# Kernel optimization log

Measured on AMD Instinct MI355X. Metric: run time of the kernel, lower is better.

Reference implementation:

```python
import jax, jax.numpy as jnp
import numpy as np

EMB = 768
HEADS = 8

def setup_inputs() -> dict:
    key = jax.random.key(0)
    ks = jax.random.split(key, 5)
    x = jax.random.normal(ks[0], (8, 2048, EMB), dtype=jnp.float32)
    s = 1.0 / np.sqrt(EMB)
    W_qkv = jax.random.normal(ks[1], (EMB, 3 * EMB), dtype=jnp.float32) * s
    b_qkv = jnp.zeros((3 * EMB,), dtype=jnp.float32)
    W_proj = jax.random.normal(ks[2], (EMB, EMB), dtype=jnp.float32) * s
    b_proj = jnp.zeros((EMB,), dtype=jnp.float32)
    return {"x": x, "W_qkv": W_qkv, "b_qkv": b_qkv, "W_proj": W_proj, "b_proj": b_proj}

def reference(x, W_qkv, b_qkv, W_proj, b_proj):
    B, N, E = x.shape
    H = HEADS
    D = E // H
    qkv = x @ W_qkv + b_qkv  # [B, N, 3E]
    q, k, v = jnp.split(qkv, 3, axis=-1)
    # [B, N, E] -> [B, H, N, D]
    def heads(t):
        return t.reshape(B, N, H, D).transpose(0, 2, 1, 3)
    q, k, v = heads(q), heads(k), heads(v)
    # NOTE: original scales by 1/sqrt(emb_size), not 1/sqrt(head_dim)
    dots = jnp.einsum('bhnd,bhmd->bhnm', q, k) / jnp.sqrt(jnp.float32(E))
    attn = jax.nn.softmax(dots, axis=-1)  # dropout inactive (eval mode)
    out = jnp.einsum('bhnm,bhmd->bhnd', attn, v)
    out = out.transpose(0, 2, 1, 3).reshape(B, N, E)
    return out @ W_proj + b_proj
```

## Files before the change

### kernel.cpp

```cpp
#include <hip/hip_runtime.h>
#include <hip/hip_bf16.h>

typedef __attribute__((ext_vector_type(8))) short bf16x8;
typedef __attribute__((ext_vector_type(4))) short bf16x4;
typedef __attribute__((ext_vector_type(4))) float f32x4;
typedef __attribute__((ext_vector_type(16))) float f32x16;
typedef __attribute__((ext_vector_type(4))) unsigned int uint4v;

__device__ __forceinline__ short f2bf(float f) {
    unsigned int u = __float_as_uint(f);
    u += 0x7FFFu + ((u >> 16) & 1u);
    return (short)(u >> 16);
}

__device__ __forceinline__ unsigned cvtpk(float lo, float hi) {
    unsigned r;
    asm("v_cvt_pk_bf16_f32 %0, %1, %2" : "=v"(r) : "v"(lo), "v"(hi));
    return r;
}

__device__ __forceinline__ void gload_lds16(const void* g, void* l) {
    __builtin_amdgcn_global_load_lds(
        (const __attribute__((address_space(1))) void*)g,
        (__attribute__((address_space(3))) void*)l, 16, 0, 0);
}

__global__ __launch_bounds__(256) void cast_kernel(const float* __restrict__ in,
                                                   short* __restrict__ out, int n4) {
    int i = blockIdx.x * 256 + threadIdx.x;
    if (i >= n4) return;
    const f32x4 v = *(const f32x4*)(in + (size_t)i * 4);
    bf16x4 o;
    o[0] = f2bf(v[0]); o[1] = f2bf(v[1]); o[2] = f2bf(v[2]); o[3] = f2bf(v[3]);
    *(bf16x4*)(out + (size_t)i * 4) = o;
}

__global__ __launch_bounds__(256) void transpose_cast_kernel(const float* __restrict__ W,
                                                             short* __restrict__ WT,
                                                             int R, int C) {
    __shared__ float tile[64][65];
    const int bc = blockIdx.x * 64;
    const int br = blockIdx.y * 64;
    const int t = threadIdx.x;
#pragma unroll
    for (int i = 0; i < 16; ++i) {
        int o = t + 256 * i;
        int r = o >> 6, c = o & 63;
        tile[r][c] = W[(size_t)(br + r) * C + bc + c];
    }
    __syncthreads();
#pragma unroll
    for (int i = 0; i < 16; ++i) {
        int o = t + 256 * i;
        int c = o >> 6, r = o & 63;
        WT[(size_t)(bc + c) * R + br + r] = f2bf(tile[r][c]);
    }
}

__global__ __launch_bounds__(256, 3) void gemm1_kernel(
    const short* __restrict__ A, const short* __restrict__ BT,
    const float* __restrict__ bias,
    short* __restrict__ Qh, short* __restrict__ Kh, short* __restrict__ Vt)
{
    __shared__ short As[128][64];
    __shared__ short Bs[128][64];
    const int K = 768;
    const int t = threadIdx.x;
    const int w = t >> 6, l = t & 63;
    const int wr = w >> 1, wc = w & 1;
    const int lr = l & 15, lg = l >> 4;

    const int srow = w * 32 + (l >> 3);
    const int scol = (l & 7) * 8;
    const short* Ag = A + (size_t)blockIdx.x * 128 * K + (size_t)srow * K + scol;
    const short* Bg = BT + (size_t)blockIdx.y * 128 * K + (size_t)srow * K + scol;

    const f32x4 z4 = {0.f, 0.f, 0.f, 0.f};
    f32x4 acc[4][4];
#pragma unroll
    for (int i = 0; i < 4; ++i)
#pragma unroll
        for (int j = 0; j < 4; ++j) acc[i][j] = z4;

    for (int kt = 0; kt < K; kt += 64) {
#pragma unroll
        for (int i = 0; i < 4; ++i) {
            gload_lds16(Ag + kt + (size_t)(i * 8) * K, &As[w * 32 + i * 8][0]);
            gload_lds16(Bg + kt + (size_t)(i * 8) * K, &Bs[w * 32 + i * 8][0]);
        }
        __syncthreads();
#pragma unroll
        for (int kk = 0; kk < 2; ++kk) {
            bf16x8 af[4], bfr[4];
#pragma unroll
            for (int mi = 0; mi < 4; ++mi)
                af[mi] = *(const bf16x8*)&As[wr * 64 + mi * 16 + lr][kk * 32 + lg * 8];
#pragma unroll
            for (int ni = 0; ni < 4; ++ni)
                bfr[ni] = *(const bf16x8*)&Bs[wc * 64 + ni * 16 + lr][kk * 32 + lg * 8];
#pragma unroll
            for (int mi = 0; mi < 4; ++mi)
#pragma unroll
                for (int ni = 0; ni < 4; ++ni)
                    acc[mi][ni] = __builtin_amdgcn_mfma_f32_16x16x32_bf16(
                        af[mi], bfr[ni], acc[mi][ni], 0, 0, 0);
        }
        __syncthreads();
    }

    const float qs = 0.05205877f;
    const int rb = blockIdx.x * 128 + wr * 64;
    const int cb = blockIdx.y * 128 + wc * 64;
#pragma unroll
    for (int ni = 0; ni < 4; ++ni) {
        const int c = cb + ni * 16 + lr;
        const float bv = bias[c];
        const int which = (c >= 1536) ? 2 : (c >= 768 ? 1 : 0);
        const int cc = c - which * 768;
        const int h = cc / 96;
        const int d = cc - h * 96;
#pragma unroll
        for (int mi = 0; mi < 4; ++mi) {
            const int r0 = rb + mi * 16 + lg * 4;
            const int b = r0 >> 11, n0 = r0 & 2047;
            const int hb = b * 8 + h;
            if (which == 2) {
                bf16x4 pk;
#pragma unroll
                for (int r = 0; r < 4; ++r) pk[r] = f2bf(acc[mi][ni][r] + bv);
                *(bf16x4*)&Vt[((size_t)hb * 96 + d) * 2048 + n0] = pk;
            } else if (which == 1) {
#pragma unroll
                for (int r = 0; r < 4; ++r)
                    Kh[((size_t)hb * 2048 + n0 + r) * 96 + d] = f2bf(acc[mi][ni][r] + bv);
            } else {
#pragma unroll
                for (int r = 0; r < 4; ++r)
                    Qh[((size_t)hb * 2048 + n0 + r) * 96 + d] = f2bf((acc[mi][ni][r] + bv) * qs);
            }
        }
    }
}

__global__ __launch_bounds__(256, 2) void attn_kernel(
    const short* __restrict__ Qh, const short* __restrict__ Kh,
    const short* __restrict__ Vt, short* __restrict__ AO)
{
    __shared__ __align__(16) char smem[54272];
    short (*Ks0)[104] = (short (*)[104])smem;
    short (*Ks1)[104] = (short (*)[104])(smem + 13312);
    short (*Vs0)[72]  = (short (*)[72])(smem + 26624);
    short (*Vs1)[72]  = (short (*)[72])(smem + 40448);
    short (*Qs)[104]  = (short (*)[104])smem;
    float (*ltab)[32] = (float (*)[32])smem;

    const int t = threadIdx.x;
    const int w = t >> 6, l = t & 63;
    const int ql = l & 31, hi = l >> 5;

    const unsigned L = blockIdx.y * 16 + blockIdx.x;
    const int bh = (int)((L & 7) + 8 * (L >> 7));
    const int qt = (int)((L >> 3) & 15);

    const short* Qg = Qh + (size_t)bh * 2048 * 96 + (size_t)qt * 128 * 96;
    const short* Kg = Kh + (size_t)bh * 2048 * 96;
    const short* Vg = Vt + (size_t)bh * 96 * 2048;

    bf16x8 kreg[3], vreg[3];
#pragma unroll
    for (int i = 0; i < 3; ++i) {
        int o = t + 256 * i;
        kreg[i] = *(const bf16x8*)(Kg + 8 * (size_t)o);
        vreg[i] = *(const bf16x8*)(Vg + (size_t)(o >> 3) * 2048 + (o & 7) * 8);
    }

#pragma unroll
    for (int i = 0; i < 6; ++i) {
        int o = t + 256 * i;
        *(bf16x8*)&Qs[o / 12][(o % 12) * 8] = *(const bf16x8*)(Qg + 8 * (size_t)o);
    }
    __syncthreads();
    bf16x8 qf[6];
#pragma unroll
    for (int kk = 0; kk < 6; ++kk)
        qf[kk] = *(const bf16x8*)&Qs[w * 32 + ql][kk * 16 + hi * 8];
    __syncthreads();

#pragma unroll
    for (int i = 0; i < 3; ++i) {
        int o = t + 256 * i;
        *(bf16x8*)&Ks0[o / 12][(o % 12) * 8] = kreg[i];
        *(bf16x8*)&Vs0[o >> 3][(o & 7) * 8] = vreg[i];
    }
#pragma unroll
    for (int i = 0; i < 3; ++i) {
        int o = t + 256 * i;
        kreg[i] = *(const bf16x8*)(Kg + (size_t)64 * 96 + 8 * (size_t)o);
        vreg[i] = *(const bf16x8*)(Vg + (size_t)(o >> 3) * 2048 + 64 + (o & 7) * 8);
    }
    __syncthreads();

    f32x16 oacc[3];
#pragma unroll
    for (int i = 0; i < 3; ++i)
#pragma unroll
        for (int r = 0; r < 16; ++r) oacc[i][r] = 0.f;
    float lacc = 0.f;

    auto iter = [&](int kt, short (*rK)[104], short (*rV)[72],
                    short (*wK)[104], short (*wV)[72]) {
        if (kt < 31) {
#pragma unroll
            for (int i = 0; i < 3; ++i) {
                int o = t + 256 * i;
                *(bf16x8*)&wK[o / 12][(o % 12) * 8] = kreg[i];
                *(bf16x8*)&wV[o >> 3][(o & 7) * 8] = vreg[i];
            }
        }
        if (kt < 30) {
            const size_t koff = (size_t)(kt + 2) * 64 * 96;
            const int moff = (kt + 2) * 64;
#pragma unroll
            for (int i = 0; i < 3; ++i) {
                int o = t + 256 * i;
                kreg[i] = *(const bf16x8*)(Kg + koff + 8 * (size_t)o);
                vreg[i] = *(const bf16x8*)(Vg + (size_t)(o >> 3) * 2048 + moff + (o & 7) * 8);
            }
        }

        f32x16 sa0, sa1;
#pragma unroll
        for (int r = 0; r < 16; ++r) { sa0[r] = 0.f; sa1[r] = 0.f; }
        __builtin_amdgcn_s_setprio(1);
#pragma unroll
        for (int kk = 0; kk < 6; ++kk) {
            bf16x8 kf0 = *(const bf16x8*)&rK[ql][kk * 16 + hi * 8];
            bf16x8 kf1 = *(const bf16x8*)&rK[32 + ql][kk * 16 + hi * 8];
            sa0 = __builtin_amdgcn_mfma_f32_32x32x16_bf16(kf0, qf[kk], sa0, 0, 0, 0);
            sa1 = __builtin_amdgcn_mfma_f32_32x32x16_bf16(kf1, qf[kk], sa1, 0, 0, 0);
        }
        __builtin_amdgcn_s_setprio(0);

        bf16x8 pa[4];
#pragma unroll
        for (int mi = 0; mi < 2; ++mi) {
            float p[16];
#pragma unroll
            for (int r = 0; r < 16; ++r) {
                p[r] = __builtin_amdgcn_exp2f(mi == 0 ? sa0[r] : sa1[r]);
                lacc += p[r];
            }
            unsigned x0 = cvtpk(p[0], p[1]),  y0 = cvtpk(p[4], p[5]);
            unsigned x1 = cvtpk(p[2], p[3]),  y1 = cvtpk(p[6], p[7]);
            unsigned x2 = cvtpk(p[8], p[9]),  y2 = cvtpk(p[12], p[13]);
            unsigned x3 = cvtpk(p[10], p[11]), y3 = cvtpk(p[14], p[15]);
            asm("v_permlane32_swap_b32 %0, %1" : "+v"(x0), "+v"(y0));
            asm("v_permlane32_swap_b32 %0, %1" : "+v"(x1), "+v"(y1));
            asm("v_permlane32_swap_b32 %0, %1" : "+v"(x2), "+v"(y2));
            asm("v_permlane32_swap_b32 %0, %1" : "+v"(x3), "+v"(y3));
            uint4v uA; uA[0] = x0; uA[1] = x1; uA[2] = y0; uA[3] = y1;
            uint4v uB; uB[0] = x2; uB[1] = x3; uB[2] = y2; uB[3] = y3;
            pa[mi * 2 + 0] = __builtin_bit_cast(bf16x8, uA);
            pa[mi * 2 + 1] = __builtin_bit_cast(bf16x8, uB);
        }

        __builtin_amdgcn_s_setprio(1);
#pragma unroll
        for (int kb = 0; kb < 4; ++kb) {
#pragma unroll
            for (int db = 0; db < 3; ++db) {
                bf16x8 vf = *(const bf16x8*)&rV[db * 32 + ql][kb * 16 + hi * 8];
                oacc[db] = __builtin_amdgcn_mfma_f32_32x32x16_bf16(pa[kb], vf, oacc[db], 0, 0, 0);
            }
        }
        __builtin_amdgcn_s_setprio(0);
        __syncthreads();
    };

    for (int kt = 0; kt < 32; kt += 2) {
        iter(kt,     Ks0, Vs0, Ks1, Vs1);
        iter(kt + 1, Ks1, Vs1, Ks0, Vs0);
    }

    float lsum = lacc + __shfl_xor(lacc, 32);
    if (l < 32) ltab[w][l] = lsum;
    asm volatile("s_waitcnt lgkmcnt(0)" ::: "memory");

    float linv[16];
#pragma unroll
    for (int r = 0; r < 16; ++r) {
        const int q = (r & 3) + 8 * (r >> 2) + 4 * hi;
        linv[r] = 1.0f / ltab[w][q];
    }

    const int b = bh >> 3, h = bh & 7;
    const size_t rowbase = (size_t)b * 2048 + qt * 128 + w * 32;
#pragma unroll
    for (int db = 0; db < 3; ++db) {
#pragma unroll
        for (int r = 0; r < 16; ++r) {
            const int q = (r & 3) + 8 * (r >> 2) + 4 * hi;
            AO[(rowbase + q) * 768 + h * 96 + db * 32 + ql] = f2bf(oacc[db][r] * linv[r]);
        }
    }
}

__global__ __launch_bounds__(256, 3) void gemm2_kernel(
    const short* __restrict__ A, const short* __restrict__ BT,
    const float* __restrict__ bias, float* __restrict__ out)
{
    __shared__ short As[128][64];
    __shared__ short Bs[128][64];
    const int K = 768;
    const int t = threadIdx.x;
    const int w = t >> 6, l = t & 63;
    const int wr = w >> 1, wc = w & 1;
    const int lr = l & 15, lg = l >> 4;

    const int srow = w * 32 + (l >> 3);
    const int scol = (l & 7) * 8;
    const short* Ag = A + (size_t)blockIdx.x * 128 * K + (size_t)srow * K + scol;
    const short* Bg = BT + (size_t)blockIdx.y * 128 * K + (size_t)srow * K + scol;

    const f32x4 z4 = {0.f, 0.f, 0.f, 0.f};
    f32x4 acc[4][4];
#pragma unroll
    for (int i = 0; i < 4; ++i)
#pragma unroll
        for (int j = 0; j < 4; ++j) acc[i][j] = z4;

    for (int kt = 0; kt < K; kt += 64) {
#pragma unroll
        for (int i = 0; i < 4; ++i) {
            gload_lds16(Ag + kt + (size_t)(i * 8) * K, &As[w * 32 + i * 8][0]);
            gload_lds16(Bg + kt + (size_t)(i * 8) * K, &Bs[w * 32 + i * 8][0]);
        }
        __syncthreads();
#pragma unroll
        for (int kk = 0; kk < 2; ++kk) {
            bf16x8 af[4], bfr[4];
#pragma unroll
            for (int mi = 0; mi < 4; ++mi)
                af[mi] = *(const bf16x8*)&As[wr * 64 + mi * 16 + lr][kk * 32 + lg * 8];
#pragma unroll
            for (int ni = 0; ni < 4; ++ni)
                bfr[ni] = *(const bf16x8*)&Bs[wc * 64 + ni * 16 + lr][kk * 32 + lg * 8];
#pragma unroll
            for (int mi = 0; mi < 4; ++mi)
#pragma unroll
                for (int ni = 0; ni < 4; ++ni)
                    acc[mi][ni] = __builtin_amdgcn_mfma_f32_16x16x32_bf16(
                        af[mi], bfr[ni], acc[mi][ni], 0, 0, 0);
        }
        __syncthreads();
    }

    const int rb = blockIdx.x * 128 + wr * 64;
    const int cb = blockIdx.y * 128 + wc * 64;
#pragma unroll
    for (int ni = 0; ni < 4; ++ni) {
        const int c = cb + ni * 16 + lr;
        const float bv = bias[c];
#pragma unroll
        for (int mi = 0; mi < 4; ++mi) {
            const int r0 = rb + mi * 16 + lg * 4;
#pragma unroll
            for (int r = 0; r < 4; ++r)
                out[(size_t)(r0 + r) * 768 + c] = acc[mi][ni][r] + bv;
        }
    }
}

extern "C" void kernel_launch(void* const* d_in, const int* in_sizes, int n_in,
                              void* d_out, int out_size, void* d_ws, size_t ws_size,
                              hipStream_t stream) {
    const float* x     = (const float*)d_in[0];
    const float* Wqkv  = (const float*)d_in[1];
    const float* bqkv  = (const float*)d_in[2];
    const float* Wproj = (const float*)d_in[3];
    const float* bproj = (const float*)d_in[4];
    float* out = (float*)d_out;

    char* ws = (char*)d_ws;
    short* xb     = (short*)(ws);
    short* WqkvT  = (short*)(ws + 25165824);
    short* WprojT = (short*)(ws + 28704768);
    short* Qh     = (short*)(ws + 29884416);
    short* Kh     = (short*)(ws + 55050240);
    short* Vt     = (short*)(ws + 80216064);
    short* AO     = xb;

    cast_kernel<<<12288, 256, 0, stream>>>(x, xb, 3145728);
    transpose_cast_kernel<<<dim3(36, 12), 256, 0, stream>>>(Wqkv, WqkvT, 768, 2304);
    transpose_cast_kernel<<<dim3(12, 12), 256, 0, stream>>>(Wproj, WprojT, 768, 768);
    gemm1_kernel<<<dim3(128, 18), 256, 0, stream>>>(xb, WqkvT, bqkv, Qh, Kh, Vt);
    attn_kernel<<<dim3(16, 64), 256, 0, stream>>>(Qh, Kh, Vt, AO);
    gemm2_kernel<<<dim3(128, 6), 256, 0, stream>>>(AO, WprojT, bproj, out);
}
```

Before: 236.6 us.

## Pre-pad K and pre-tile/swizzle V in gemm1, stream via direct global-to-LDS loads

gemm1 now writes K with a 104-element padded row stride and writes V transposed into per-64-key tiles with an XOR swizzle. The attention kernel can then stage K, V and Q straight into LDS with global_load_lds DMA instead of going through registers. The score/softmax/PV loop is split into two 32-key halves to lower register pressure, and the occupancy hint rises from 2 to 3 blocks per CU, with LDS shrunk to fit. The Vt workspace offset moves to make room for the larger padded K buffer. In exchange, the padded K layout costs extra global memory, and there is now only a single buffer of prefetch lead.

```diff
diff --git a/kernel.cpp b/kernel.cpp
--- a/kernel.cpp
+++ b/kernel.cpp
@@ -128,11 +128,13 @@
                 bf16x4 pk;
 #pragma unroll
                 for (int r = 0; r < 4; ++r) pk[r] = f2bf(acc[mi][ni][r] + bv);
-                *(bf16x4*)&Vt[((size_t)hb * 96 + d) * 2048 + n0] = pk;
+                const int ktile = n0 >> 6;
+                const int s = (((n0 & 63) >> 3) ^ (d & 7));
+                *(bf16x4*)&Vt[((size_t)(hb * 32 + ktile) * 96 + d) * 64 + s * 8 + (n0 & 7)] = pk;
             } else if (which == 1) {
 #pragma unroll
                 for (int r = 0; r < 4; ++r)
-                    Kh[((size_t)hb * 2048 + n0 + r) * 96 + d] = f2bf(acc[mi][ni][r] + bv);
+                    Kh[((size_t)hb * 2048 + n0 + r) * 104 + d] = f2bf(acc[mi][ni][r] + bv);
             } else {
 #pragma unroll
                 for (int r = 0; r < 4; ++r)
@@ -142,16 +144,16 @@
     }
 }
 
-__global__ __launch_bounds__(256, 2) void attn_kernel(
+__global__ __launch_bounds__(256, 3) void attn_kernel(
     const short* __restrict__ Qh, const short* __restrict__ Kh,
     const short* __restrict__ Vt, short* __restrict__ AO)
 {
-    __shared__ __align__(16) char smem[54272];
-    short (*Ks0)[104] = (short (*)[104])smem;
-    short (*Ks1)[104] = (short (*)[104])(smem + 13312);
-    short (*Vs0)[72]  = (short (*)[72])(smem + 26624);
-    short (*Vs1)[72]  = (short (*)[72])(smem + 40448);
-    short (*Qs)[104]  = (short (*)[104])smem;
+    __shared__ __align__(16) char smem[51200];
+    short (*K0)[104] = (short (*)[104])smem;
+    short (*K1)[104] = (short (*)[104])(smem + 13312);
+    short* V0 = (short*)(smem + 26624);
+    short* V1 = (short*)(smem + 38912);
+    short (*Qs)[96] = (short (*)[96])smem;
     float (*ltab)[32] = (float (*)[32])smem;
 
     const int t = threadIdx.x;
@@ -162,22 +164,14 @@
     const int bh = (int)((L & 7) + 8 * (L >> 7));
     const int qt = (int)((L >> 3) & 15);
 
-    const short* Qg = Qh + (size_t)bh * 2048 * 96 + (size_t)qt * 128 * 96;
-    const short* Kg = Kh + (size_t)bh * 2048 * 96;
-    const short* Vg = Vt + (size_t)bh * 96 * 2048;
-
-    bf16x8 kreg[3], vreg[3];
-#pragma unroll
-    for (int i = 0; i < 3; ++i) {
-        int o = t + 256 * i;
-        kreg[i] = *(const bf16x8*)(Kg + 8 * (size_t)o);
-        vreg[i] = *(const bf16x8*)(Vg + (size_t)(o >> 3) * 2048 + (o & 7) * 8);
-    }
-
-#pragma unroll
-    for (int i = 0; i < 6; ++i) {
-        int o = t + 256 * i;
-        *(bf16x8*)&Qs[o / 12][(o % 12) * 8] = *(const bf16x8*)(Qg + 8 * (size_t)o);
+    const short* Qg  = Qh + ((size_t)bh * 2048 + (size_t)qt * 128) * 96;
+    const short* Kgp = Kh + (size_t)bh * 2048 * 104;
+    const short* Vgt = Vt + (size_t)bh * 32 * 6144;
+
+#pragma unroll
+    for (int j = 0; j < 6; ++j) {
+        const int idx = j * 4 + w;
+        gload_lds16(Qg + idx * 512 + l * 8, smem + idx * 1024);
     }
     __syncthreads();
     bf16x8 qf[6];
@@ -186,18 +180,25 @@
         qf[kk] = *(const bf16x8*)&Qs[w * 32 + ql][kk * 16 + hi * 8];
     __syncthreads();
 
-#pragma unroll
-    for (int i = 0; i < 3; ++i) {
-        int o = t + 256 * i;
-        *(bf16x8*)&Ks0[o / 12][(o % 12) * 8] = kreg[i];
-        *(bf16x8*)&Vs0[o >> 3][(o & 7) * 8] = vreg[i];
-    }
-#pragma unroll
-    for (int i = 0; i < 3; ++i) {
-        int o = t + 256 * i;
-        kreg[i] = *(const bf16x8*)(Kg + (size_t)64 * 96 + 8 * (size_t)o);
-        vreg[i] = *(const bf16x8*)(Vg + (size_t)(o >> 3) * 2048 + 64 + (o & 7) * 8);
-    }
+    auto stageK = [&](int kt, short (*wK)[104]) {
+        const short* s = Kgp + kt * 6656 + l * 8;
+#pragma unroll
+        for (int j = 0; j < 4; ++j) {
+            const int idx = j * 4 + w;
+            if (idx < 13) gload_lds16(s + idx * 512, (char*)wK + idx * 1024);
+        }
+    };
+    auto stageV = [&](int kt, short* wV) {
+        const short* s = Vgt + kt * 6144 + l * 8;
+#pragma unroll
+        for (int j = 0; j < 3; ++j) {
+            const int idx = j * 4 + w;
+            gload_lds16(s + idx * 512, (char*)wV + idx * 1024);
+        }
+    };
+
+    stageK(0, K0);
+    stageV(0, V0);
     __syncthreads();
 
     f32x16 oacc[3];
@@ -207,52 +208,32 @@
         for (int r = 0; r < 16; ++r) oacc[i][r] = 0.f;
     float lacc = 0.f;
 
-    auto iter = [&](int kt, short (*rK)[104], short (*rV)[72],
-                    short (*wK)[104], short (*wV)[72]) {
-        if (kt < 31) {
-#pragma unroll
-            for (int i = 0; i < 3; ++i) {
-                int o = t + 256 * i;
-                *(bf16x8*)&wK[o / 12][(o % 12) * 8] = kreg[i];
-                *(bf16x8*)&wV[o >> 3][(o & 7) * 8] = vreg[i];
+    auto iter = [&](int kt, short (*rK)[104], const short* rV,
+                    short (*wK)[104], short* wV) {
+        if (kt < 31) { stageK(kt + 1, wK); stageV(kt + 1, wV); }
+
+#pragma unroll
+        for (int h = 0; h < 2; ++h) {
+            f32x16 sa;
+#pragma unroll
+            for (int r = 0; r < 16; ++r) sa[r] = 0.f;
+            __builtin_amdgcn_s_setprio(1);
+#pragma unroll
+            for (int kk = 0; kk < 6; ++kk) {
+                bf16x8 kf = *(const bf16x8*)&rK[h * 32 + ql][kk * 16 + hi * 8];
+                sa = __builtin_amdgcn_mfma_f32_32x32x16_bf16(kf, qf[kk], sa, 0, 0, 0);
             }
-        }
-        if (kt < 30) {
-            const size_t koff = (size_t)(kt + 2) * 64 * 96;
-            const int moff = (kt + 2) * 64;
-#pragma unroll
-            for (int i = 0; i < 3; ++i) {
-                int o = t + 256 * i;
-                kreg[i] = *(const bf16x8*)(Kg + koff + 8 * (size_t)o);
-                vreg[i] = *(const bf16x8*)(Vg + (size_t)(o >> 3) * 2048 + moff + (o & 7) * 8);
-            }
-        }
-
-        f32x16 sa0, sa1;
-#pragma unroll
-        for (int r = 0; r < 16; ++r) { sa0[r] = 0.f; sa1[r] = 0.f; }
-        __builtin_amdgcn_s_setprio(1);
-#pragma unroll
-        for (int kk = 0; kk < 6; ++kk) {
-            bf16x8 kf0 = *(const bf16x8*)&rK[ql][kk * 16 + hi * 8];
-            bf16x8 kf1 = *(const bf16x8*)&rK[32 + ql][kk * 16 + hi * 8];
-            sa0 = __builtin_amdgcn_mfma_f32_32x32x16_bf16(kf0, qf[kk], sa0, 0, 0, 0);
-            sa1 = __builtin_amdgcn_mfma_f32_32x32x16_bf16(kf1, qf[kk], sa1, 0, 0, 0);
-        }
-        __builtin_amdgcn_s_setprio(0);
-
-        bf16x8 pa[4];
-#pragma unroll
-        for (int mi = 0; mi < 2; ++mi) {
+            __builtin_amdgcn_s_setprio(0);
+
             float p[16];
 #pragma unroll
             for (int r = 0; r < 16; ++r) {
-                p[r] = __builtin_amdgcn_exp2f(mi == 0 ? sa0[r] : sa1[r]);
+                p[r] = __builtin_amdgcn_exp2f(sa[r]);
                 lacc += p[r];
             }
-            unsigned x0 = cvtpk(p[0], p[1]),  y0 = cvtpk(p[4], p[5]);
-            unsigned x1 = cvtpk(p[2], p[3]),  y1 = cvtpk(p[6], p[7]);
-            unsigned x2 = cvtpk(p[8], p[9]),  y2 = cvtpk(p[12], p[13]);
+            unsigned x0 = cvtpk(p[0], p[1]),   y0 = cvtpk(p[4], p[5]);
+            unsigned x1 = cvtpk(p[2], p[3]),   y1 = cvtpk(p[6], p[7]);
+            unsigned x2 = cvtpk(p[8], p[9]),   y2 = cvtpk(p[12], p[13]);
             unsigned x3 = cvtpk(p[10], p[11]), y3 = cvtpk(p[14], p[15]);
             asm("v_permlane32_swap_b32 %0, %1" : "+v"(x0), "+v"(y0));
             asm("v_permlane32_swap_b32 %0, %1" : "+v"(x1), "+v"(y1));
@@ -260,26 +241,29 @@
             asm("v_permlane32_swap_b32 %0, %1" : "+v"(x3), "+v"(y3));
             uint4v uA; uA[0] = x0; uA[1] = x1; uA[2] = y0; uA[3] = y1;
             uint4v uB; uB[0] = x2; uB[1] = x3; uB[2] = y2; uB[3] = y3;
-            pa[mi * 2 + 0] = __builtin_bit_cast(bf16x8, uA);
-            pa[mi * 2 + 1] = __builtin_bit_cast(bf16x8, uB);
-        }
-
-        __builtin_amdgcn_s_setprio(1);
-#pragma unroll
-        for (int kb = 0; kb < 4; ++kb) {
-#pragma unroll
-            for (int db = 0; db < 3; ++db) {
-                bf16x8 vf = *(const bf16x8*)&rV[db * 32 + ql][kb * 16 + hi * 8];
-                oacc[db] = __builtin_amdgcn_mfma_f32_32x32x16_bf16(pa[kb], vf, oacc[db], 0, 0, 0);
+            bf16x8 pa0 = __builtin_bit_cast(bf16x8, uA);
+            bf16x8 pa1 = __builtin_bit_cast(bf16x8, uB);
+
+            __builtin_amdgcn_s_setprio(1);
+#pragma unroll
+            for (int kb = 0; kb < 2; ++kb) {
+                const int c = (h * 2 + kb) * 2 + hi;
+                const bf16x8 paf = kb ? pa1 : pa0;
+#pragma unroll
+                for (int db = 0; db < 3; ++db) {
+                    const int row = db * 32 + ql;
+                    bf16x8 vf = *(const bf16x8*)&rV[row * 64 + ((c ^ (row & 7)) << 3)];
+                    oacc[db] = __builtin_amdgcn_mfma_f32_32x32x16_bf16(paf, vf, oacc[db], 0, 0, 0);
+                }
             }
-        }
-        __builtin_amdgcn_s_setprio(0);
+            __builtin_amdgcn_s_setprio(0);
+        }
         __syncthreads();
     };
 
     for (int kt = 0; kt < 32; kt += 2) {
-        iter(kt,     Ks0, Vs0, Ks1, Vs1);
-        iter(kt + 1, Ks1, Vs1, Ks0, Vs0);
+        iter(kt,     K0, V0, K1, V1);
+        iter(kt + 1, K1, V1, K0, V0);
     }
 
     float lsum = lacc + __shfl_xor(lacc, 32);
@@ -293,14 +277,14 @@
         linv[r] = 1.0f / ltab[w][q];
     }
 
-    const int b = bh >> 3, h = bh & 7;
+    const int b = bh >> 3, h2 = bh & 7;
     const size_t rowbase = (size_t)b * 2048 + qt * 128 + w * 32;
 #pragma unroll
     for (int db = 0; db < 3; ++db) {
 #pragma unroll
         for (int r = 0; r < 16; ++r) {
             const int q = (r & 3) + 8 * (r >> 2) + 4 * hi;
-            AO[(rowbase + q) * 768 + h * 96 + db * 32 + ql] = f2bf(oacc[db][r] * linv[r]);
+            AO[(rowbase + q) * 768 + h2 * 96 + db * 32 + ql] = f2bf(oacc[db][r] * linv[r]);
         }
     }
 }
@@ -387,7 +371,7 @@
     short* WprojT = (short*)(ws + 28704768);
     short* Qh     = (short*)(ws + 29884416);
     short* Kh     = (short*)(ws + 55050240);
-    short* Vt     = (short*)(ws + 80216064);
+    short* Vt     = (short*)(ws + 82313216);
     short* AO     = xb;
 
     cast_kernel<<<12288, 256, 0, stream>>>(x, xb, 3145728);
```

Result: no change. 239.5 us (+1.2%).
